# Performance work log

Measured on AMD Instinct MI355X. Metric: run time of the kernel, lower is better.

Reference implementation:

```python
import jax, jax.numpy as jnp
import numpy as np

INPUT_SIZE = 256
HIDDEN_SIZE = 256


def setup_inputs() -> dict:
    key = jax.random.key(0)
    k_x, k_wxh, k_whh = jax.random.split(key, 3)
    x = jax.random.normal(k_x, (64, 2048, INPUT_SIZE), dtype=jnp.float32)
    # torch nn.Linear weights: [out_features, in_features]
    W_xh = jax.random.normal(k_wxh, (HIDDEN_SIZE, INPUT_SIZE), dtype=jnp.float32) / np.sqrt(INPUT_SIZE)
    W_hh = jax.random.normal(k_whh, (HIDDEN_SIZE, HIDDEN_SIZE), dtype=jnp.float32) / np.sqrt(HIDDEN_SIZE)
    b_h = jnp.zeros((HIDDEN_SIZE,), dtype=jnp.float32)
    return {"x": x, "W_xh": W_xh, "W_hh": W_hh, "b_h": b_h}


def reference(x, W_xh, W_hh, b_h):
    # x: [B, T, D]; h_t = relu(x_t @ W_xh^T + h_{t-1} @ W_hh^T + b_h)
    B, T, _ = x.shape
    # Precompute input projection for all timesteps in one GEMM (same math).
    xproj = jnp.einsum('btd,hd->bth', x, W_xh) + b_h  # [B, T, H]

    def step(h, xp_t):
        h_new = jax.nn.relu(xp_t + h @ W_hh.T)
        return h_new, h_new

    h0 = jnp.zeros((B, HIDDEN_SIZE), dtype=x.dtype)
    # scan over time axis: move T to leading dim
    _, hs = jax.lax.scan(step, h0, jnp.swapaxes(xproj, 0, 1))  # hs: [T, B, H]
    return jnp.swapaxes(hs, 0, 1)  # [B, T, H]
```

## Files before the change

### kernel.cpp

```cpp
#include <hip/hip_runtime.h>

#define BATCH 64
#define SEQT  2048
#define DIM   256
#define HID   256
#define NSEG  16
#define SEGT  128

typedef _Float16 half_t;
typedef _Float16 half2_t __attribute__((ext_vector_type(2)));
typedef _Float16 half4_t __attribute__((ext_vector_type(4)));
typedef _Float16 half8_t __attribute__((ext_vector_type(8)));
typedef float    float4_t __attribute__((ext_vector_type(4)));

__device__ __forceinline__ half8_t cvt8(float4_t a, float4_t b) {
  half8_t r;
  r[0] = (half_t)a[0]; r[1] = (half_t)a[1]; r[2] = (half_t)a[2]; r[3] = (half_t)a[3];
  r[4] = (half_t)b[0]; r[5] = (half_t)b[1]; r[6] = (half_t)b[2]; r[7] = (half_t)b[3];
  return r;
}
#define H2X(v, c) __builtin_shufflevector((v), (v), 2*(c), 2*(c)+1)

template<int CTRL>
__device__ __forceinline__ float dpp_mov(float a) {
  int t = __builtin_amdgcn_mov_dpp(__builtin_bit_cast(int, a), CTRL, 0xF, 0xF, true);
  return __builtin_bit_cast(float, t);
}

#define RNN_BAR() asm volatile("s_waitcnt lgkmcnt(0)\n\ts_barrier" ::: "memory")

__device__ __forceinline__ void poll_flag(const unsigned int* f) {
  if (threadIdx.x == 0) {
    while (__hip_atomic_load(f, __ATOMIC_ACQUIRE, __HIP_MEMORY_SCOPE_AGENT) == 0u)
      __builtin_amdgcn_s_sleep(2);
  }
  __syncthreads();
}

__global__ __launch_bounds__(256) void prep_kernel(
    const float* __restrict__ W, half_t* __restrict__ Wh,
    unsigned int* __restrict__ flags)
{
  const int i = (blockIdx.x * 256 + threadIdx.x) * 4;
  float4_t v = *(const float4_t*)(W + i);
  half4_t o; o[0]=(half_t)v[0]; o[1]=(half_t)v[1]; o[2]=(half_t)v[2]; o[3]=(half_t)v[3];
  *(half4_t*)(Wh + i) = o;
  if (blockIdx.x == 0) {
    flags[threadIdx.x]       = 0u;
    flags[threadIdx.x + 256] = 0u;
    flags[threadIdx.x + 512] = 0u;
    flags[threadIdx.x + 768] = 0u;
  }
}

#define RNN_STEP(U, XQ)                                                        \
  {                                                                            \
    const int t = t4 + (U);                                                    \
    const int tp = (t + 4 < T) ? (t + 4) : (T - 1);                            \
    float xnew = outp[(long)tp * HID];                                         \
    half8_t hv[4];                                                             \
    _Pragma("unroll")                                                          \
    for (int s = 0; s < 4; ++s)                                                \
      hv[s] = *(const half8_t*)(hraw[(U) & 1] + rb + 16 * s);                  \
    float a0 = 0.f, a1 = 0.f, a2 = 0.f, a3 = 0.f;                              \
    _Pragma("unroll")                                                          \
    for (int s = 0; s < 4; ++s) {                                              \
      a0 = __builtin_amdgcn_fdot2(H2X(w8[0][s], 0), H2X(hv[s], 0), a0, false); \
      a0 = __builtin_amdgcn_fdot2(H2X(w8[0][s], 1), H2X(hv[s], 1), a0, false); \
      a0 = __builtin_amdgcn_fdot2(H2X(w8[0][s], 2), H2X(hv[s], 2), a0, false); \
      a0 = __builtin_amdgcn_fdot2(H2X(w8[0][s], 3), H2X(hv[s], 3), a0, false); \
      a1 = __builtin_amdgcn_fdot2(H2X(w8[1][s], 0), H2X(hv[s], 0), a1, false); \
      a1 = __builtin_amdgcn_fdot2(H2X(w8[1][s], 1), H2X(hv[s], 1), a1, false); \
      a1 = __builtin_amdgcn_fdot2(H2X(w8[1][s], 2), H2X(hv[s], 2), a1, false); \
      a1 = __builtin_amdgcn_fdot2(H2X(w8[1][s], 3), H2X(hv[s], 3), a1, false); \
      a2 = __builtin_amdgcn_fdot2(H2X(w8[2][s], 0), H2X(hv[s], 0), a2, false); \
      a2 = __builtin_amdgcn_fdot2(H2X(w8[2][s], 1), H2X(hv[s], 1), a2, false); \
      a2 = __builtin_amdgcn_fdot2(H2X(w8[2][s], 2), H2X(hv[s], 2), a2, false); \
      a2 = __builtin_amdgcn_fdot2(H2X(w8[2][s], 3), H2X(hv[s], 3), a2, false); \
      a3 = __builtin_amdgcn_fdot2(H2X(w8[3][s], 0), H2X(hv[s], 0), a3, false); \
      a3 = __builtin_amdgcn_fdot2(H2X(w8[3][s], 1), H2X(hv[s], 1), a3, false); \
      a3 = __builtin_amdgcn_fdot2(H2X(w8[3][s], 2), H2X(hv[s], 2), a3, false); \
      a3 = __builtin_amdgcn_fdot2(H2X(w8[3][s], 3), H2X(hv[s], 3), a3, false); \
    }                                                                          \
    float r0 = kA ? a0 : a2;                                                   \
    float r1 = kA ? a1 : a3;                                                   \
    float b0 = (kA ? a2 : a0) + dpp_mov<0x141>(r0);                            \
    float b1 = (kA ? a3 : a1) + dpp_mov<0x141>(r1);                            \
    float rB = kB ? b0 : b1;                                                   \
    float c  = (kB ? b1 : b0) + dpp_mov<0x4E>(rB);                             \
    float fin = c + dpp_mov<0xB1>(c);                                          \
    float y = fmaxf(fin + (XQ), 0.f);                                          \
    outp[(long)t * HID] = y;                                                   \
    *(half_t*)(hraw[((U) & 1) ^ 1] + hwb) = (half_t)y;                         \
    XQ = xnew;                                                                 \
    RNN_BAR();                                                                 \
  }

__global__ __launch_bounds__(512, 1) void fused_kernel(
    const float* __restrict__ x, const half_t* __restrict__ Wxh16,
    const float* __restrict__ Whh, const float* __restrict__ bh,
    float* __restrict__ out, unsigned int* __restrict__ flags, int T)
{
  if (blockIdx.x >= 64) {
    const int b = blockIdx.x - 64;
    const int k = b >> 6;
    const int c = b & 63;
    const int lane = threadIdx.x & 63;
    const int w = threadIdx.x >> 6;
    const int r16 = lane & 15;
    const int kg = lane >> 4;
    const long m0 = ((long)c * NSEG + k) * SEGT;

    half8_t bfr[2][8];
    float bb[2];
    #pragma unroll
    for (int i = 0; i < 2; ++i) {
      const int nt = w * 2 + i;
      const half_t* wr = Wxh16 + (nt * 16 + r16) * (long)DIM + kg * 8;
      #pragma unroll
      for (int kf = 0; kf < 8; ++kf)
        bfr[i][kf] = *(const half8_t*)(wr + kf * 32);
      bb[i] = bh[nt * 16 + r16];
    }
    #pragma unroll 1
    for (int mi = 0; mi < 8; ++mi) {
      const long mrow = m0 + mi * 16;
      half8_t a[8];
      const float* xr = x + (mrow + r16) * (long)DIM + kg * 8;
      #pragma unroll
      for (int kf = 0; kf < 8; ++kf) {
        float4_t x0 = *(const float4_t*)(xr + kf * 32);
        float4_t x1 = *(const float4_t*)(xr + kf * 32 + 4);
        a[kf] = cvt8(x0, x1);
      }
      #pragma unroll
      for (int i = 0; i < 2; ++i) {
        float4_t acc = {bb[i], bb[i], bb[i], bb[i]};
        #pragma unroll
        for (int kf = 0; kf < 8; ++kf)
          acc = __builtin_amdgcn_mfma_f32_16x16x32_f16(a[kf], bfr[i][kf], acc, 0, 0, 0);
        float* op = out + (mrow + kg * 4) * (long)HID + (w * 2 + i) * 16 + r16;
        #pragma unroll
        for (int r = 0; r < 4; ++r) op[(long)r * HID] = acc[r];
      }
    }
    __syncthreads();
    if (threadIdx.x == 0)
      __hip_atomic_store(flags + ((c << 4) | k), 1u, __ATOMIC_RELEASE,
                         __HIP_MEMORY_SCOPE_AGENT);
    return;
  }

  __builtin_amdgcn_s_setprio(3);

  __shared__ alignas(128) unsigned char hraw[2][8 * 80];

  const int chain = blockIdx.x;
  const int tid = threadIdx.x;
  const int l   = tid & 63;
  const int w   = tid >> 6;
  const int g   = l & 7;
  const int j0  = w * 32 + (l >> 3) * 4;
  const int rb  = g * 80;
  const int jown = j0 + ((l >> 1) & 3);
  const int hwb = ((jown >> 5) * 80 + (jown & 31) * 2);
  const bool kA = (l & 4) != 0;
  const bool kB = (l & 2) != 0;
  const unsigned int* fl = flags + (chain << 4);
  float* outp = out + (long)chain * SEQT * HID + jown;

  half8_t w8[4][4];
  #pragma unroll
  for (int i = 0; i < 4; ++i) {
    const float* wr = Whh + (long)(j0 + i) * HID + g * 32;
    #pragma unroll
    for (int s = 0; s < 4; ++s) {
      float4_t v0 = *(const float4_t*)(wr + s * 8);
      float4_t v1 = *(const float4_t*)(wr + s * 8 + 4);
      w8[i][s] = cvt8(v0, v1);
    }
  }

  if (tid < 160) ((float*)hraw[0])[tid] = 0.f;

  poll_flag(fl + 0);
  float xq0 = outp[0L * HID];
  float xq1 = outp[1L * HID];
  float xq2 = outp[2L * HID];
  float xq3 = outp[3L * HID];
  RNN_BAR();

  #pragma unroll 1
  for (int seg = 0; seg < NSEG; ++seg) {
    const int ps = (seg + 1 < NSEG) ? (seg + 1) : (NSEG - 1);
    poll_flag(fl + ps);
    const int tend = seg * SEGT + SEGT;
    #pragma unroll 1
    for (int t4 = seg * SEGT; t4 < tend; t4 += 4) {
      RNN_STEP(0, xq0)
      RNN_STEP(1, xq1)
      RNN_STEP(2, xq2)
      RNN_STEP(3, xq3)
    }
  }
}

__global__ __launch_bounds__(256) void xproj_kernel(
    const float* __restrict__ x, const float* __restrict__ Wxh,
    const float* __restrict__ bh, float* __restrict__ out)
{
  const int lane = threadIdx.x & 63;
  const int wave = threadIdx.x >> 6;
  const int r16  = lane & 15;
  const int kg   = lane >> 4;
  const long m0  = (long)blockIdx.x * 64 + wave * 16;

  half8_t a[8];
  const float* xr = x + (m0 + r16) * (long)DIM + kg * 8;
  #pragma unroll
  for (int kf = 0; kf < 8; ++kf) {
    float4_t x0 = *(const float4_t*)(xr + kf * 32);
    float4_t x1 = *(const float4_t*)(xr + kf * 32 + 4);
    a[kf] = cvt8(x0, x1);
  }
  for (int nt = 0; nt < 16; ++nt) {
    const float* wr = Wxh + (nt * 16 + r16) * (long)DIM + kg * 8;
    float bb = bh[nt * 16 + r16];
    float4_t acc = {bb, bb, bb, bb};
    #pragma unroll
    for (int kf = 0; kf < 8; ++kf) {
      float4_t w0 = *(const float4_t*)(wr + kf * 32);
      float4_t w1 = *(const float4_t*)(wr + kf * 32 + 4);
      acc = __builtin_amdgcn_mfma_f32_16x16x32_f16(a[kf], cvt8(w0, w1), acc, 0, 0, 0);
    }
    float* op = out + (m0 + kg * 4) * (long)HID + nt * 16 + r16;
    #pragma unroll
    for (int r = 0; r < 4; ++r) op[(long)r * HID] = acc[r];
  }
}

__global__ __launch_bounds__(512, 1) void rnn_kernel(
    const float* __restrict__ Whh, float* __restrict__ out, int T)
{
  __shared__ alignas(128) unsigned char hraw[2][8 * 80];

  const int tid = threadIdx.x;
  const int l   = tid & 63;
  const int w   = tid >> 6;
  const int g   = l & 7;
  const int j0  = w * 32 + (l >> 3) * 4;
  const int rb  = g * 80;
  const int jown = j0 + ((l >> 1) & 3);
  const int hwb = ((jown >> 5) * 80 + (jown & 31) * 2);
  const bool kA = (l & 4) != 0;
  const bool kB = (l & 2) != 0;
  float* outp = out + (long)blockIdx.x * SEQT * HID + jown;

  half8_t w8[4][4];
  #pragma unroll
  for (int i = 0; i < 4; ++i) {
    const float* wr = Whh + (long)(j0 + i) * HID + g * 32;
    #pragma unroll
    for (int s = 0; s < 4; ++s) {
      float4_t v0 = *(const float4_t*)(wr + s * 8);
      float4_t v1 = *(const float4_t*)(wr + s * 8 + 4);
      w8[i][s] = cvt8(v0, v1);
    }
  }
  if (tid < 160) ((float*)hraw[0])[tid] = 0.f;

  float xq0 = outp[0L * HID];
  float xq1 = outp[1L * HID];
  float xq2 = outp[2L * HID];
  float xq3 = outp[3L * HID];
  RNN_BAR();

  #pragma unroll 1
  for (int t4 = 0; t4 < T; t4 += 4) {
    RNN_STEP(0, xq0)
    RNN_STEP(1, xq1)
    RNN_STEP(2, xq2)
    RNN_STEP(3, xq3)
  }
}

extern "C" void kernel_launch(void* const* d_in, const int* in_sizes, int n_in,
                              void* d_out, int out_size, void* d_ws, size_t ws_size,
                              hipStream_t stream) {
  const float* x   = (const float*)d_in[0];
  const float* Wxh = (const float*)d_in[1];
  const float* Whh = (const float*)d_in[2];
  const float* bh  = (const float*)d_in[3];
  float* out = (float*)d_out;

  const size_t wh_bytes = (size_t)DIM * HID * sizeof(half_t);
  const size_t need = wh_bytes + 4096;

  if (ws_size >= need) {
    half_t* Wh = (half_t*)d_ws;
    unsigned int* flags = (unsigned int*)((char*)d_ws + wh_bytes);
    prep_kernel<<<dim3((DIM * HID) / 1024), dim3(256), 0, stream>>>(Wxh, Wh, flags);
    fused_kernel<<<dim3(64 + BATCH * NSEG), dim3(512), 0, stream>>>(
        x, Wh, Whh, bh, out, flags, SEQT);
  } else {
    xproj_kernel<<<dim3((BATCH * SEQT) / 64), dim3(256), 0, stream>>>(x, Wxh, bh, out);
    rnn_kernel<<<dim3(BATCH), dim3(512), 0, stream>>>(Whh, out, SEQT);
  }
}
```

Measured before the change: 888.3 us.

## Compute recurrent matvec with MFMA on four waves instead of fdot2 reductions

The recurrent step now uses MFMA 16x16x32 instructions, with the W_hh tiles held in registers across four waves. The hidden state is broadcast as a B operand, and only column 0 of each result is used. This replaces the per-lane fdot2 plus DPP cross-lane reduction over eight waves, and halves the number of waves that do real work. The other four waves only take part in barriers. The trade-off is that 15 of 16 MFMA columns are wasted, MFMA latency on the serial chain may be longer than the dot-product path, and the s_setprio hint is dropped.

```diff
diff --git a/kernel.cpp b/kernel.cpp
--- a/kernel.cpp
+++ b/kernel.cpp
@@ -50,6 +50,175 @@
     flags[threadIdx.x + 256] = 0u;
     flags[threadIdx.x + 512] = 0u;
     flags[threadIdx.x + 768] = 0u;
+  }
+}
+
+#define RNN_MSTEP(U, XQ)                                                       \
+  {                                                                            \
+    const int t = t2 + (U);                                                    \
+    const int tp = (t + 2 < T) ? (t + 2) : (T - 1);                            \
+    float4_t xn0 = *(const float4_t*)(outp + (long)tp * HID + n0);             \
+    float4_t xn1 = *(const float4_t*)(outp + (long)tp * HID + n1);             \
+    float4_t xn2 = *(const float4_t*)(outp + (long)tp * HID + n2);             \
+    float4_t xn3 = *(const float4_t*)(outp + (long)tp * HID + n3);             \
+    half8_t bh8[8];                                                            \
+    _Pragma("unroll")                                                          \
+    for (int kf = 0; kf < 8; ++kf)                                             \
+      bh8[kf] = *(const half8_t*)(hby[(U)] + kf * 64 + q * 16);                \
+    float4_t ac0 = XQ[0], ac1 = XQ[1], ac2 = XQ[2], ac3 = XQ[3];               \
+    _Pragma("unroll")                                                          \
+    for (int kf = 0; kf < 8; ++kf) {                                           \
+      ac0 = __builtin_amdgcn_mfma_f32_16x16x32_f16(aw[0][kf], bh8[kf], ac0, 0, 0, 0); \
+      ac1 = __builtin_amdgcn_mfma_f32_16x16x32_f16(aw[1][kf], bh8[kf], ac1, 0, 0, 0); \
+      ac2 = __builtin_amdgcn_mfma_f32_16x16x32_f16(aw[2][kf], bh8[kf], ac2, 0, 0, 0); \
+      ac3 = __builtin_amdgcn_mfma_f32_16x16x32_f16(aw[3][kf], bh8[kf], ac3, 0, 0, 0); \
+    }                                                                          \
+    ac0[0]=fmaxf(ac0[0],0.f); ac0[1]=fmaxf(ac0[1],0.f);                        \
+    ac0[2]=fmaxf(ac0[2],0.f); ac0[3]=fmaxf(ac0[3],0.f);                        \
+    ac1[0]=fmaxf(ac1[0],0.f); ac1[1]=fmaxf(ac1[1],0.f);                        \
+    ac1[2]=fmaxf(ac1[2],0.f); ac1[3]=fmaxf(ac1[3],0.f);                        \
+    ac2[0]=fmaxf(ac2[0],0.f); ac2[1]=fmaxf(ac2[1],0.f);                        \
+    ac2[2]=fmaxf(ac2[2],0.f); ac2[3]=fmaxf(ac2[3],0.f);                        \
+    ac3[0]=fmaxf(ac3[0],0.f); ac3[1]=fmaxf(ac3[1],0.f);                        \
+    ac3[2]=fmaxf(ac3[2],0.f); ac3[3]=fmaxf(ac3[3],0.f);                        \
+    if (act16) {                                                               \
+      *(float4_t*)(outp + (long)t * HID + n0) = ac0;                           \
+      *(float4_t*)(outp + (long)t * HID + n1) = ac1;                           \
+      *(float4_t*)(outp + (long)t * HID + n2) = ac2;                           \
+      *(float4_t*)(outp + (long)t * HID + n3) = ac3;                           \
+      half4_t h0, h1, h2, h3;                                                  \
+      h0[0]=(half_t)ac0[0]; h0[1]=(half_t)ac0[1]; h0[2]=(half_t)ac0[2]; h0[3]=(half_t)ac0[3]; \
+      h1[0]=(half_t)ac1[0]; h1[1]=(half_t)ac1[1]; h1[2]=(half_t)ac1[2]; h1[3]=(half_t)ac1[3]; \
+      h2[0]=(half_t)ac2[0]; h2[1]=(half_t)ac2[1]; h2[2]=(half_t)ac2[2]; h2[3]=(half_t)ac2[3]; \
+      h3[0]=(half_t)ac3[0]; h3[1]=(half_t)ac3[1]; h3[2]=(half_t)ac3[2]; h3[3]=(half_t)ac3[3]; \
+      *(half4_t*)(hby[(U) ^ 1] + n0 * 2) = h0;                                 \
+      *(half4_t*)(hby[(U) ^ 1] + n1 * 2) = h1;                                 \
+      *(half4_t*)(hby[(U) ^ 1] + n2 * 2) = h2;                                 \
+      *(half4_t*)(hby[(U) ^ 1] + n3 * 2) = h3;                                 \
+    }                                                                          \
+    XQ[0] = xn0; XQ[1] = xn1; XQ[2] = xn2; XQ[3] = xn3;                        \
+    RNN_BAR();                                                                 \
+  }
+
+__global__ __launch_bounds__(512, 1) void fused_kernel(
+    const float* __restrict__ x, const half_t* __restrict__ Wxh16,
+    const float* __restrict__ Whh, const float* __restrict__ bh,
+    float* __restrict__ out, unsigned int* __restrict__ flags, int T)
+{
+  if (blockIdx.x >= 64) {
+    const int b = blockIdx.x - 64;
+    const int k = b >> 6;
+    const int c = b & 63;
+    const int lane = threadIdx.x & 63;
+    const int w = threadIdx.x >> 6;
+    const int r16 = lane & 15;
+    const int kg = lane >> 4;
+    const long m0 = ((long)c * NSEG + k) * SEGT;
+
+    half8_t bfr[2][8];
+    float bb[2];
+    #pragma unroll
+    for (int i = 0; i < 2; ++i) {
+      const int nt = w * 2 + i;
+      const half_t* wr = Wxh16 + (nt * 16 + r16) * (long)DIM + kg * 8;
+      #pragma unroll
+      for (int kf = 0; kf < 8; ++kf)
+        bfr[i][kf] = *(const half8_t*)(wr + kf * 32);
+      bb[i] = bh[nt * 16 + r16];
+    }
+    #pragma unroll 1
+    for (int mi = 0; mi < 8; ++mi) {
+      const long mrow = m0 + mi * 16;
+      half8_t a[8];
+      const float* xr = x + (mrow + r16) * (long)DIM + kg * 8;
+      #pragma unroll
+      for (int kf = 0; kf < 8; ++kf) {
+        float4_t x0 = *(const float4_t*)(xr + kf * 32);
+        float4_t x1 = *(const float4_t*)(xr + kf * 32 + 4);
+        a[kf] = cvt8(x0, x1);
+      }
+      #pragma unroll
+      for (int i = 0; i < 2; ++i) {
+        float4_t acc = {bb[i], bb[i], bb[i], bb[i]};
+        #pragma unroll
+        for (int kf = 0; kf < 8; ++kf)
+          acc = __builtin_amdgcn_mfma_f32_16x16x32_f16(a[kf], bfr[i][kf], acc, 0, 0, 0);
+        float* op = out + (mrow + kg * 4) * (long)HID + (w * 2 + i) * 16 + r16;
+        #pragma unroll
+        for (int r = 0; r < 4; ++r) op[(long)r * HID] = acc[r];
+      }
+    }
+    __syncthreads();
+    if (threadIdx.x == 0)
+      __hip_atomic_store(flags + ((c << 4) | k), 1u, __ATOMIC_RELEASE,
+                         __HIP_MEMORY_SCOPE_AGENT);
+    return;
+  }
+
+  __shared__ alignas(16) half_t hl[2][HID];
+
+  const int chain = threadIdx.x >= 0 ? blockIdx.x : 0;
+  const int tid = threadIdx.x;
+  const int l   = tid & 63;
+  const int w   = tid >> 6;
+  const unsigned int* fl = flags + (chain << 4);
+
+  if (w >= 4) {
+    __syncthreads();
+    RNN_BAR();
+    for (int seg = 0; seg < NSEG; ++seg) {
+      __syncthreads();
+      for (int i = 0; i < SEGT / 2; ++i) { RNN_BAR(); RNN_BAR(); }
+    }
+    return;
+  }
+
+  const int r16 = l & 15;
+  const int q   = l >> 4;
+  const bool act16 = (r16 == 0);
+  const int n0 = (4 * w + 0) * 16 + q * 4;
+  const int n1 = (4 * w + 1) * 16 + q * 4;
+  const int n2 = (4 * w + 2) * 16 + q * 4;
+  const int n3 = (4 * w + 3) * 16 + q * 4;
+  unsigned char* hby[2] = { (unsigned char*)hl[0], (unsigned char*)hl[1] };
+  float* outp = out + (long)chain * SEQT * HID;
+
+  half8_t aw[4][8];
+  #pragma unroll
+  for (int i = 0; i < 4; ++i) {
+    const float* wr = Whh + (long)((4 * w + i) * 16 + r16) * HID + q * 8;
+    #pragma unroll
+    for (int kf = 0; kf < 8; ++kf) {
+      float4_t v0 = *(const float4_t*)(wr + kf * 32);
+      float4_t v1 = *(const float4_t*)(wr + kf * 32 + 4);
+      aw[i][kf] = cvt8(v0, v1);
+    }
+  }
+
+  if (tid < 64) ((half4_t*)hl[0])[tid] = half4_t{0, 0, 0, 0};
+
+  poll_flag(fl + 0);
+  float4_t xqe[4], xqo[4];
+  xqe[0] = *(const float4_t*)(outp + 0L * HID + n0);
+  xqe[1] = *(const float4_t*)(outp + 0L * HID + n1);
+  xqe[2] = *(const float4_t*)(outp + 0L * HID + n2);
+  xqe[3] = *(const float4_t*)(outp + 0L * HID + n3);
+  xqo[0] = *(const float4_t*)(outp + 1L * HID + n0);
+  xqo[1] = *(const float4_t*)(outp + 1L * HID + n1);
+  xqo[2] = *(const float4_t*)(outp + 1L * HID + n2);
+  xqo[3] = *(const float4_t*)(outp + 1L * HID + n3);
+  RNN_BAR();
+
+  #pragma unroll 1
+  for (int seg = 0; seg < NSEG; ++seg) {
+    const int ps = (seg + 1 < NSEG) ? (seg + 1) : (NSEG - 1);
+    poll_flag(fl + ps);
+    const int tend = seg * SEGT + SEGT;
+    #pragma unroll 1
+    for (int t2 = seg * SEGT; t2 < tend; t2 += 2) {
+      RNN_MSTEP(0, xqe)
+      RNN_MSTEP(1, xqo)
+    }
   }
 }
 
@@ -96,115 +265,6 @@
     RNN_BAR();                                                                 \
   }
 
-__global__ __launch_bounds__(512, 1) void fused_kernel(
-    const float* __restrict__ x, const half_t* __restrict__ Wxh16,
-    const float* __restrict__ Whh, const float* __restrict__ bh,
-    float* __restrict__ out, unsigned int* __restrict__ flags, int T)
-{
-  if (blockIdx.x >= 64) {
-    const int b = blockIdx.x - 64;
-    const int k = b >> 6;
-    const int c = b & 63;
-    const int lane = threadIdx.x & 63;
-    const int w = threadIdx.x >> 6;
-    const int r16 = lane & 15;
-    const int kg = lane >> 4;
-    const long m0 = ((long)c * NSEG + k) * SEGT;
-
-    half8_t bfr[2][8];
-    float bb[2];
-    #pragma unroll
-    for (int i = 0; i < 2; ++i) {
-      const int nt = w * 2 + i;
-      const half_t* wr = Wxh16 + (nt * 16 + r16) * (long)DIM + kg * 8;
-      #pragma unroll
-      for (int kf = 0; kf < 8; ++kf)
-        bfr[i][kf] = *(const half8_t*)(wr + kf * 32);
-      bb[i] = bh[nt * 16 + r16];
-    }
-    #pragma unroll 1
-    for (int mi = 0; mi < 8; ++mi) {
-      const long mrow = m0 + mi * 16;
-      half8_t a[8];
-      const float* xr = x + (mrow + r16) * (long)DIM + kg * 8;
-      #pragma unroll
-      for (int kf = 0; kf < 8; ++kf) {
-        float4_t x0 = *(const float4_t*)(xr + kf * 32);
-        float4_t x1 = *(const float4_t*)(xr + kf * 32 + 4);
-        a[kf] = cvt8(x0, x1);
-      }
-      #pragma unroll
-      for (int i = 0; i < 2; ++i) {
-        float4_t acc = {bb[i], bb[i], bb[i], bb[i]};
-        #pragma unroll
-        for (int kf = 0; kf < 8; ++kf)
-          acc = __builtin_amdgcn_mfma_f32_16x16x32_f16(a[kf], bfr[i][kf], acc, 0, 0, 0);
-        float* op = out + (mrow + kg * 4) * (long)HID + (w * 2 + i) * 16 + r16;
-        #pragma unroll
-        for (int r = 0; r < 4; ++r) op[(long)r * HID] = acc[r];
-      }
-    }
-    __syncthreads();
-    if (threadIdx.x == 0)
-      __hip_atomic_store(flags + ((c << 4) | k), 1u, __ATOMIC_RELEASE,
-                         __HIP_MEMORY_SCOPE_AGENT);
-    return;
-  }
-
-  __builtin_amdgcn_s_setprio(3);
-
-  __shared__ alignas(128) unsigned char hraw[2][8 * 80];
-
-  const int chain = blockIdx.x;
-  const int tid = threadIdx.x;
-  const int l   = tid & 63;
-  const int w   = tid >> 6;
-  const int g   = l & 7;
-  const int j0  = w * 32 + (l >> 3) * 4;
-  const int rb  = g * 80;
-  const int jown = j0 + ((l >> 1) & 3);
-  const int hwb = ((jown >> 5) * 80 + (jown & 31) * 2);
-  const bool kA = (l & 4) != 0;
-  const bool kB = (l & 2) != 0;
-  const unsigned int* fl = flags + (chain << 4);
-  float* outp = out + (long)chain * SEQT * HID + jown;
-
-  half8_t w8[4][4];
-  #pragma unroll
-  for (int i = 0; i < 4; ++i) {
-    const float* wr = Whh + (long)(j0 + i) * HID + g * 32;
-    #pragma unroll
-    for (int s = 0; s < 4; ++s) {
-      float4_t v0 = *(const float4_t*)(wr + s * 8);
-      float4_t v1 = *(const float4_t*)(wr + s * 8 + 4);
-      w8[i][s] = cvt8(v0, v1);
-    }
-  }
-
-  if (tid < 160) ((float*)hraw[0])[tid] = 0.f;
-
-  poll_flag(fl + 0);
-  float xq0 = outp[0L * HID];
-  float xq1 = outp[1L * HID];
-  float xq2 = outp[2L * HID];
-  float xq3 = outp[3L * HID];
-  RNN_BAR();
-
-  #pragma unroll 1
-  for (int seg = 0; seg < NSEG; ++seg) {
-    const int ps = (seg + 1 < NSEG) ? (seg + 1) : (NSEG - 1);
-    poll_flag(fl + ps);
-    const int tend = seg * SEGT + SEGT;
-    #pragma unroll 1
-    for (int t4 = seg * SEGT; t4 < tend; t4 += 4) {
-      RNN_STEP(0, xq0)
-      RNN_STEP(1, xq1)
-      RNN_STEP(2, xq2)
-      RNN_STEP(3, xq3)
-    }
-  }
-}
-
 __global__ __launch_bounds__(256) void xproj_kernel(
     const float* __restrict__ x, const float* __restrict__ Wxh,
     const float* __restrict__ bh, float* __restrict__ out)
```

Result: slower. 1.235 ms (+39.0%).
